# Optimization experiments

Measured on AMD Instinct MI355X. Metric: run time of the kernel, lower is better.

## Reference

```python
import jax, jax.numpy as jnp
import numpy as np

NUM_HEAD = 16
SIZE_PER_HEAD = 64
D_MODEL = NUM_HEAD * SIZE_PER_HEAD
BATCH = 4
SEQ = 2048
MASK_VAL = 1e10  # module uses 10000000000.0 for the causal mask


def setup_inputs() -> dict:
    key = jax.random.key(0)
    ks = jax.random.split(key, 11)
    s = 1.0 / np.sqrt(D_MODEL)
    return {
        "q": jax.random.normal(ks[0], (BATCH, SEQ, D_MODEL), jnp.float32),
        "k": jax.random.normal(ks[1], (BATCH, SEQ, D_MODEL), jnp.float32),
        "v": jax.random.normal(ks[2], (BATCH, SEQ, D_MODEL), jnp.float32),
        "WQ": jax.random.normal(ks[3], (D_MODEL, D_MODEL), jnp.float32) * s,
        "WQ_bias": jax.random.normal(ks[4], (D_MODEL,), jnp.float32) * 0.02,
        "WK": jax.random.normal(ks[5], (D_MODEL, D_MODEL), jnp.float32) * s,
        "WK_bias": jax.random.normal(ks[6], (D_MODEL,), jnp.float32) * 0.02,
        "WV": jax.random.normal(ks[7], (D_MODEL, D_MODEL), jnp.float32) * s,
        "WV_bias": jax.random.normal(ks[8], (D_MODEL,), jnp.float32) * 0.02,
        "WO": jax.random.normal(ks[9], (D_MODEL, D_MODEL), jnp.float32) * s,
        "WO_bias": jax.random.normal(ks[10], (D_MODEL,), jnp.float32) * 0.02,
    }


def _split_heads(x):
    # [B, S, H*D] -> [B, H, S, D]
    b, s, _ = x.shape
    return x.reshape(b, s, NUM_HEAD, SIZE_PER_HEAD).transpose(0, 2, 1, 3)


def reference(q, k, v, WQ, WQ_bias, WK, WK_bias, WV, WV_bias, WO, WO_bias):
    Q = _split_heads(q @ WQ + WQ_bias)  # [B,H,M,D]
    Kh = _split_heads(k @ WK + WK_bias)  # [B,H,N,D]
    Vh = _split_heads(v @ WV + WV_bias)  # [B,H,N,D]

    A = jnp.einsum('bhmd,bhnd->bhmn', Q, Kh)
    # causal mask (is_right=True): subtract 1e10 on strict upper triangle,
    # applied BEFORE the 1/sqrt(d) scale, exactly as the original.
    m, n = A.shape[-2], A.shape[-1]
    causal = jnp.triu(jnp.ones((m, n), A.dtype), k=1) * jnp.asarray(MASK_VAL, A.dtype)
    A = A - causal
    A = jax.nn.softmax(A / np.sqrt(SIZE_PER_HEAD).astype(np.float32), axis=-1)

    O = jnp.einsum('bhmn,bhnd->bhmd', A, Vh)  # [B,H,M,D]
    b, h, s, d = O.shape
    O = O.transpose(0, 2, 1, 3).reshape(b, s, h * d)
    return O @ WO + WO_bias
```

## Files before the change

### kernel.cpp

```cpp
#include <hip/hip_runtime.h>
#include <hip/hip_bf16.h>

typedef unsigned short u16;
typedef __attribute__((ext_vector_type(8))) short bf8_t;
typedef __attribute__((ext_vector_type(4))) float f4_t;
typedef __attribute__((ext_vector_type(2))) unsigned u32x2_t;
typedef __attribute__((ext_vector_type(4))) unsigned u32x4_t;

#define D_MODEL 1024
#define SEQ     2048
#define NHEAD   16
#define DH      64
#define MTOK    8192
#define ELEMS_PER_MAT 8388608

__device__ __forceinline__ u16 f2b(float x) {
    unsigned u = __float_as_uint(x);
    u += 0x7fffu + ((u >> 16) & 1u);
    return (u16)(u >> 16);
}

__device__ __forceinline__ unsigned pkrn(float lo, float hi) {
    __hip_bfloat162 h = __float22bfloat162_rn(make_float2(lo, hi));
    unsigned r;
    __builtin_memcpy(&r, &h, 4);
    return r;
}

__device__ __forceinline__ float ex2(float x) {
    float r;
    asm("v_exp_f32 %0, %1" : "=v"(r) : "v"(x));
    return r;
}

__device__ __forceinline__ void gl_lds16(const void* g, void* l) {
    __builtin_amdgcn_global_load_lds(
        (const __attribute__((address_space(1))) void*)g,
        (__attribute__((address_space(3))) void*)l, 16, 0, 0);
}

struct P3 { const float* p[3]; };
__global__ void cvt_in3(P3 src, u16* __restrict__ dst) {
    int z = blockIdx.y;
    const float* s = src.p[z];
    u16* d = dst + (size_t)z * ELEMS_PER_MAT;
    int i = blockIdx.x * 256 + threadIdx.x;
    const float4* s4 = (const float4*)s;
    float4 a = s4[i * 2];
    float4 b = s4[i * 2 + 1];
    bf8_t o;
    o[0] = (short)f2b(a.x); o[1] = (short)f2b(a.y);
    o[2] = (short)f2b(a.z); o[3] = (short)f2b(a.w);
    o[4] = (short)f2b(b.x); o[5] = (short)f2b(b.y);
    o[6] = (short)f2b(b.z); o[7] = (short)f2b(b.w);
    *(bf8_t*)&d[(size_t)i * 8] = o;
}

#define QSCALE 0.1803368801111244f
struct W4 { const float* w[4]; };
__global__ void cvt_wt(W4 wa, u16* __restrict__ wt) {
    int z = blockIdx.z;
    const float* W = wa.w[z];
    u16* Wt = wt + (size_t)z * 1048576;
    float scale = (z == 0) ? QSCALE : 1.0f;
    __shared__ float tl[64][65];
    int t = threadIdx.x;
    int bx = blockIdx.x, by = blockIdx.y;
#pragma unroll
    for (int i = 0; i < 16; i++) {
        int e = i * 256 + t;
        int row = e >> 6, col = e & 63;
        tl[row][col] = W[(size_t)(by * 64 + row) * 1024 + bx * 64 + col];
    }
    __syncthreads();
#pragma unroll
    for (int i = 0; i < 16; i++) {
        int e = i * 256 + t;
        int row = e >> 6, col = e & 63;
        Wt[(size_t)(bx * 64 + row) * 1024 + by * 64 + col] = f2b(tl[col][row] * scale);
    }
}

struct B4 { const float* b[4]; };
__global__ void cvt_bias(B4 ba, float* __restrict__ dst) {
    int t = threadIdx.x;
    for (int z = 0; z < 4; z++) {
        float sc = (z == 0) ? QSCALE : 1.0f;
        for (int i = t; i < 1024; i += 256) dst[z * 1024 + i] = ba.b[z][i] * sc;
    }
}

template <int MODE>
__global__ __launch_bounds__(256, 2) void gemm_k(const u16* __restrict__ Ab,
                                                 const u16* __restrict__ Btb,
                                                 const float* __restrict__ biasb,
                                                 void* __restrict__ out0,
                                                 u16* __restrict__ outV) {
    int z = blockIdx.z;
    const u16* A  = Ab  + (size_t)z * ELEMS_PER_MAT;
    const u16* Bt = Btb + (size_t)z * 1048576;
    const float* bias = biasb + z * 1024;
    bool vswap = (MODE == 3) && (z == 2);

    int bid = blockIdx.y * 64 + blockIdx.x;
    int xcd = bid & 7, seq = bid >> 3;
    int tm = xcd * 8 + (seq & 7);
    int tn = seq >> 3;
    int t = threadIdx.x;
    int wid = t >> 6, lane = t & 63;
    int wm = wid >> 1, wn = wid & 1;
    int la = lane & 15, lh = lane >> 4;

    __shared__ __align__(16) char smem[65536];

    f4_t acc[4][4];
#pragma unroll
    for (int m = 0; m < 4; m++)
#pragma unroll
        for (int n = 0; n < 4; n++) acc[m][n] = (f4_t){0.f, 0.f, 0.f, 0.f};

    const u16* Agb = A  + (size_t)(tm * 128) * 1024;
    const u16* Bgb = Bt + (size_t)(tn * 128) * 1024;

    int ch0 = wid * 64 + lane;
    int so0 = (lh ^ (la & 7)) * 8;
    int so1 = so0 ^ 32;

    auto stage = [&](int k0, int b) {
#pragma unroll
        for (int i = 0; i < 4; i++) {
            int ch = ch0 + i * 256;
            int row = ch >> 3, c8 = ch & 7;
            int srcc = (c8 ^ (row & 7)) * 8;
            gl_lds16(Agb + (size_t)row * 1024 + k0 + srcc,
                     smem + b * 32768 + (size_t)(i * 4 + wid) * 1024);
            gl_lds16(Bgb + (size_t)row * 1024 + k0 + srcc,
                     smem + b * 32768 + 16384 + (size_t)(i * 4 + wid) * 1024);
        }
    };

    stage(0, 0);
    __syncthreads();
    int cur = 0;
    for (int kt = 0; kt < 16; kt++) {
        if (kt + 1 < 16) stage((kt + 1) * 64, cur ^ 1);
        const u16* As = (const u16*)(smem + cur * 32768);
        const u16* Bs = (const u16*)(smem + cur * 32768 + 16384);
#pragma unroll
        for (int ks = 0; ks < 2; ks++) {
            int so = ks ? so1 : so0;
            bf8_t af[4], bf[4];
#pragma unroll
            for (int m = 0; m < 4; m++)
                af[m] = *(const bf8_t*)&As[(wm * 64 + m * 16 + la) * 64 + so];
#pragma unroll
            for (int n = 0; n < 4; n++)
                bf[n] = *(const bf8_t*)&Bs[(wn * 64 + n * 16 + la) * 64 + so];
            if (vswap) {
#pragma unroll
                for (int m = 0; m < 4; m++)
#pragma unroll
                    for (int n = 0; n < 4; n++)
                        acc[m][n] = __builtin_amdgcn_mfma_f32_16x16x32_bf16(bf[n], af[m], acc[m][n], 0, 0, 0);
            } else {
#pragma unroll
                for (int m = 0; m < 4; m++)
#pragma unroll
                    for (int n = 0; n < 4; n++)
                        acc[m][n] = __builtin_amdgcn_mfma_f32_16x16x32_bf16(af[m], bf[n], acc[m][n], 0, 0, 0);
            }
        }
        __syncthreads();
        cur ^= 1;
    }

    int lh4 = lh * 4;
    int bq = tm >> 4;
    int sloc = (tm & 15) * 128;

    if (MODE == 1) {
        float* ef = (float*)smem;
#pragma unroll
        for (int m = 0; m < 4; m++) {
            int row = wm * 64 + m * 16 + lh4;
#pragma unroll
            for (int n = 0; n < 4; n++) {
                int cb = wn * 64 + n * 16;
                float bv = bias[tn * 128 + cb + la];
#pragma unroll
                for (int r = 0; r < 4; r++)
                    ef[(row + r) * 128 + cb + la] = acc[m][n][r] + bv;
            }
        }
        __syncthreads();
        float* og = (float*)out0;
#pragma unroll
        for (int p = 0; p < 16; p++) {
            int e = t * 4 + p * 1024;
            int row = e >> 7, col = e & 127;
            f4_t v = *(const f4_t*)&ef[e];
            *(f4_t*)&og[(size_t)(tm * 128 + row) * 1024 + tn * 128 + col] = v;
        }
    } else if (vswap) {
        u16* eb = (u16*)smem;
#pragma unroll
        for (int m = 0; m < 4; m++) {
            int s = wm * 64 + m * 16 + la;
#pragma unroll
            for (int n = 0; n < 4; n++) {
                int cb = wn * 64 + n * 16 + lh4;
#pragma unroll
                for (int r = 0; r < 4; r++)
                    eb[(cb + r) * 128 + s] = f2b(acc[m][n][r] + bias[tn * 128 + cb + r]);
            }
        }
        __syncthreads();
#pragma unroll
        for (int p = 0; p < 8; p++) {
            int col = (t >> 4) + p * 16;
            int chunk = (t & 15) * 8;
            int h = tn * 2 + (col >> 6), d = col & 63;
            bf8_t v = *(const bf8_t*)&eb[col * 128 + chunk];
            *(bf8_t*)&outV[(((size_t)(bq * NHEAD + h)) * DH + d) * SEQ + sloc + chunk] = v;
        }
    } else {
        u16* eb = (u16*)smem;
#pragma unroll
        for (int m = 0; m < 4; m++) {
            int row = wm * 64 + m * 16 + lh4;
#pragma unroll
            for (int n = 0; n < 4; n++) {
                int cb = wn * 64 + n * 16;
                float bv = bias[tn * 128 + cb + la];
#pragma unroll
                for (int r = 0; r < 4; r++)
                    eb[wn * 8192 + (row + r) * 64 + n * 16 + la] = f2b(acc[m][n][r] + bv);
            }
        }
        __syncthreads();
        u16* outz = (u16*)out0 + (size_t)z * ELEMS_PER_MAT;
        size_t gbase = ((size_t)(bq * NHEAD + tn * 2) * SEQ + sloc) * DH;
#pragma unroll
        for (int p = 0; p < 8; p++) {
            int e = t * 8 + p * 2048;
            int hl = e >> 13, inner = e & 8191;
            bf8_t v = *(const bf8_t*)&eb[e];
            *(bf8_t*)&outz[gbase + (size_t)hl * SEQ * DH + inner] = v;
        }
    }
}

__global__ __launch_bounds__(256, 4) void attn(const u16* __restrict__ Qp,
                                               const u16* __restrict__ Kp,
                                               const u16* __restrict__ Vt,
                                               u16* __restrict__ ctx) {
    int id = blockIdx.x;
    int qt = 31 - (id >> 6);
    int bh = id & 63;
    int t = threadIdx.x, wid = t >> 6, lane = t & 63;
    int la = lane & 15, lh = lane >> 4;
    int lh4 = lh * 4;
    int lh8 = lh * 8;
    int q0 = qt * 64;

    const u16* Qb = Qp + (size_t)bh * SEQ * DH;
    const u16* Kb = Kp + (size_t)bh * SEQ * DH;
    const u16* Vb = Vt + (size_t)bh * DH * SEQ;

    __shared__ __align__(16) u16 Kl[2 * 4096];
    __shared__ __align__(16) u16 Vl[2 * 4096];

    int qrow = q0 + wid * 16 + la;
    bf8_t qf0 = *(const bf8_t*)&Qb[(size_t)qrow * DH + lh8];
    bf8_t qf1 = *(const bf8_t*)&Qb[(size_t)qrow * DH + 32 + lh8];

    bf8_t onesf;
#pragma unroll
    for (int i = 0; i < 8; i++) onesf[i] = (short)0x3F80;

    float m = -1e30f;
    f4_t o[4] = {};
    f4_t o5  = {};

    int s0 = t, s1 = t + 256;
    int rr0 = s0 >> 3, rr1 = s1 >> 3;
    int ck0 = ((s0 & 7) ^ (rr0 & 7)) * 8;
    int ck1 = ((s1 & 7) ^ (rr1 & 7)) * 8;
    int key0 = (rr0 & 0x23) | ((rr0 & 0x0C) << 1) | ((rr0 & 0x10) >> 2);
    int key1 = (rr1 & 0x23) | ((rr1 & 0x0C) << 1) | ((rr1 & 0x10) >> 2);
    const u16* kp0 = Kb + (size_t)key0 * DH + ck0;
    const u16* kp1 = Kb + (size_t)key1 * DH + ck1;
    const u16* vp0 = Vb + (size_t)rr0 * SEQ + ck0;
    const u16* vp1 = Vb + (size_t)rr1 * SEQ + ck1;

    int ntiles = qt + 1;
    auto stage = [&](int tile, int b) {
        int kv0 = tile * 64;
        gl_lds16(kp0 + (size_t)kv0 * DH, (char*)Kl + b * 8192 + wid * 1024);
        gl_lds16(kp1 + (size_t)kv0 * DH, (char*)Kl + b * 8192 + 4096 + wid * 1024);
        gl_lds16(vp0 + kv0,              (char*)Vl + b * 8192 + wid * 1024);
        gl_lds16(vp1 + kv0,              (char*)Vl + b * 8192 + 4096 + wid * 1024);
    };
    stage(0, 0);

    int csA = (lh ^ (la & 7)) * 8;
    int csB = ((4 | lh) ^ (la & 7)) * 8;

    for (int tkv = 0; tkv < ntiles; ++tkv) {
        __syncthreads();
        if (tkv + 1 < ntiles) stage(tkv + 1, (tkv + 1) & 1);
        const u16* Kd = Kl + (tkv & 1) * 4096;
        const u16* Vd = Vl + (tkv & 1) * 4096;

        bool diag = (tkv == qt);
        int ntmax = diag ? ((wid < 2) ? 2 : 4) : 4;

        f4_t st[4];
        __builtin_amdgcn_s_setprio(1);
#pragma unroll
        for (int nt = 0; nt < 4; nt++) {
            if (nt < ntmax) {
                bf8_t kf0 = *(const bf8_t*)&Kd[(nt * 16 + la) * 64 + csA];
                bf8_t kf1 = *(const bf8_t*)&Kd[(nt * 16 + la) * 64 + csB];
                f4_t a = (f4_t){0.f, 0.f, 0.f, 0.f};
                a = __builtin_amdgcn_mfma_f32_16x16x32_bf16(kf0, qf0, a, 0, 0, 0);
                a = __builtin_amdgcn_mfma_f32_16x16x32_bf16(kf1, qf1, a, 0, 0, 0);
                if (diag) {
                    int kbase = ((nt >> 1) << 5) + (lh << 3) + ((nt & 1) << 2);
#pragma unroll
                    for (int r = 0; r < 4; r++)
                        if (kbase + r > wid * 16 + la) a[r] = -1e30f;
                }
                st[nt] = a;
            } else {
                st[nt] = (f4_t){-1e30f, -1e30f, -1e30f, -1e30f};
            }
        }
        __builtin_amdgcn_s_setprio(0);

        float mloc = -3e38f;
#pragma unroll
        for (int nt = 0; nt < 4; nt++)
            if (nt < ntmax) {
                mloc = fmaxf(mloc, fmaxf(fmaxf(st[nt][0], st[nt][1]),
                                         fmaxf(st[nt][2], st[nt][3])));
            }
        mloc = fmaxf(mloc, __shfl_xor(mloc, 16));
        mloc = fmaxf(mloc, __shfl_xor(mloc, 32));
        if (!__all(mloc <= m + 8.0f)) {
            float mnew = fmaxf(m, mloc);
            float alpha = ex2(m - mnew);
#pragma unroll
            for (int dm = 0; dm < 4; dm++) o[dm] *= alpha;
            o5 *= alpha;
            m = mnew;
        }

#pragma unroll
        for (int nt = 0; nt < 4; nt++) {
#pragma unroll
            for (int r = 0; r < 4; r++)
                st[nt][r] = ex2(st[nt][r] - m);
        }

        __builtin_amdgcn_s_setprio(1);
#pragma unroll
        for (int kk = 0; kk < 2; kk++) {
            if (2 * kk < ntmax) {
                u32x4_t pw;
                pw[0] = pkrn(st[2 * kk][0], st[2 * kk][1]);
                pw[1] = pkrn(st[2 * kk][2], st[2 * kk][3]);
                pw[2] = pkrn(st[2 * kk + 1][0], st[2 * kk + 1][1]);
                pw[3] = pkrn(st[2 * kk + 1][2], st[2 * kk + 1][3]);
                bf8_t pf;
                __builtin_memcpy(&pf, &pw, 16);
                int cs = kk ? csB : csA;
#pragma unroll
                for (int dm = 0; dm < 4; dm++) {
                    bf8_t vf = *(const bf8_t*)&Vd[(dm * 16 + la) * 64 + cs];
                    o[dm] = __builtin_amdgcn_mfma_f32_16x16x32_bf16(vf, pf, o[dm], 0, 0, 0);
                }
                o5 = __builtin_amdgcn_mfma_f32_16x16x32_bf16(onesf, pf, o5, 0, 0, 0);
            }
        }
        __builtin_amdgcn_s_setprio(0);
    }

    float inv = 1.0f / o5[0];
    int b = bh >> 4, h = bh & 15;
    size_t base = ((size_t)(b * SEQ + qrow)) * D_MODEL + h * DH;
#pragma unroll
    for (int dm = 0; dm < 4; dm++) {
        u32x2_t w;
        w[0] = pkrn(o[dm][0] * inv, o[dm][1] * inv);
        w[1] = pkrn(o[dm][2] * inv, o[dm][3] * inv);
        *(u32x2_t*)&ctx[base + dm * 16 + lh4] = w;
    }
}

extern "C" void kernel_launch(void* const* d_in, const int* in_sizes, int n_in,
                              void* d_out, int out_size, void* d_ws, size_t ws_size,
                              hipStream_t stream) {
    const float* q   = (const float*)d_in[0];
    const float* k   = (const float*)d_in[1];
    const float* v   = (const float*)d_in[2];
    const float* WQ  = (const float*)d_in[3];
    const float* WQb = (const float*)d_in[4];
    const float* WK  = (const float*)d_in[5];
    const float* WKb = (const float*)d_in[6];
    const float* WV  = (const float*)d_in[7];
    const float* WVb = (const float*)d_in[8];
    const float* WO  = (const float*)d_in[9];
    const float* WOb = (const float*)d_in[10];

    char* ws = (char*)d_ws;
    u16*   qkv_bf = (u16*)(ws);
    u16*   Wt     = (u16*)(ws + 50331648);
    float* biasws = (float*)(ws + 58720256);
    u16*   QKVp   = (u16*)(ws + 58736640);
    u16*   Vt_    = (u16*)(ws + 109068288);
    u16*   ctx    = (u16*)(ws + 125845504);

    P3 p3; p3.p[0] = q; p3.p[1] = k; p3.p[2] = v;
    cvt_in3<<<dim3(4096, 3), 256, 0, stream>>>(p3, qkv_bf);

    W4 w4; w4.w[0] = WQ; w4.w[1] = WK; w4.w[2] = WV; w4.w[3] = WO;
    cvt_wt<<<dim3(16, 16, 4), 256, 0, stream>>>(w4, Wt);
    B4 b4; b4.b[0] = WQb; b4.b[1] = WKb; b4.b[2] = WVb; b4.b[3] = WOb;
    cvt_bias<<<1, 256, 0, stream>>>(b4, biasws);

    gemm_k<3><<<dim3(64, 8, 3), 256, 0, stream>>>(qkv_bf, Wt, biasws, QKVp, Vt_);

    attn<<<dim3(2048), 256, 0, stream>>>(QKVp, QKVp + ELEMS_PER_MAT, Vt_, ctx);

    gemm_k<1><<<dim3(64, 8, 1), 256, 0, stream>>>(ctx, Wt + 3 * 1048576,
                                                  biasws + 3 * 1024, d_out, nullptr);
}
```

Measured before the change: 183.2 us.

## Fuse fp32-to-bf16 input conversion into QKV projection GEMM A-tile loads

Removes the separate kernel that converted q/k/v from fp32 to bf16. The QKV GEMM now loads fp32 A tiles into registers, converts and packs them to bf16, and writes them swizzled into LDS after the MFMA work of the current tile. This drops one launch and the round trip of the bf16 copy through global memory. In exchange the GEMM reads twice as many bytes per A tile, uses more registers, and loses the direct global-to-LDS load path for A.

New measurement: 181.3 us. Within noise of the previous version (-1.1%).

```diff
diff --git a/kernel.cpp b/kernel.cpp
--- a/kernel.cpp
+++ b/kernel.cpp
@@ -40,21 +40,6 @@
 }
 
 struct P3 { const float* p[3]; };
-__global__ void cvt_in3(P3 src, u16* __restrict__ dst) {
-    int z = blockIdx.y;
-    const float* s = src.p[z];
-    u16* d = dst + (size_t)z * ELEMS_PER_MAT;
-    int i = blockIdx.x * 256 + threadIdx.x;
-    const float4* s4 = (const float4*)s;
-    float4 a = s4[i * 2];
-    float4 b = s4[i * 2 + 1];
-    bf8_t o;
-    o[0] = (short)f2b(a.x); o[1] = (short)f2b(a.y);
-    o[2] = (short)f2b(a.z); o[3] = (short)f2b(a.w);
-    o[4] = (short)f2b(b.x); o[5] = (short)f2b(b.y);
-    o[6] = (short)f2b(b.z); o[7] = (short)f2b(b.w);
-    *(bf8_t*)&d[(size_t)i * 8] = o;
-}
 
 #define QSCALE 0.1803368801111244f
 struct W4 { const float* w[4]; };
@@ -91,13 +76,14 @@
 }
 
 template <int MODE>
-__global__ __launch_bounds__(256, 2) void gemm_k(const u16* __restrict__ Ab,
+__global__ __launch_bounds__(256, 2) void gemm_k(P3 a3,
+                                                 const u16* __restrict__ Ab16,
                                                  const u16* __restrict__ Btb,
                                                  const float* __restrict__ biasb,
                                                  void* __restrict__ out0,
                                                  u16* __restrict__ outV) {
     int z = blockIdx.z;
-    const u16* A  = Ab  + (size_t)z * ELEMS_PER_MAT;
+    const float* Af = (MODE == 3) ? a3.p[z] : nullptr;
     const u16* Bt = Btb + (size_t)z * 1048576;
     const float* bias = biasb + z * 1024;
     bool vswap = (MODE == 3) && (z == 2);
@@ -119,14 +105,40 @@
 #pragma unroll
         for (int n = 0; n < 4; n++) acc[m][n] = (f4_t){0.f, 0.f, 0.f, 0.f};
 
-    const u16* Agb = A  + (size_t)(tm * 128) * 1024;
     const u16* Bgb = Bt + (size_t)(tn * 128) * 1024;
 
     int ch0 = wid * 64 + lane;
     int so0 = (lh ^ (la & 7)) * 8;
     int so1 = so0 ^ 32;
 
-    auto stage = [&](int k0, int b) {
+    f4_t areg[4][2];
+
+    auto aload = [&](int k0) {
+#pragma unroll
+        for (int i = 0; i < 4; i++) {
+            int ch = ch0 + i * 256;
+            int row = ch >> 3, c8 = ch & 7;
+            const float* src = Af + (size_t)(tm * 128 + row) * 1024 + k0 + c8 * 8;
+            areg[i][0] = *(const f4_t*)src;
+            areg[i][1] = *(const f4_t*)(src + 4);
+        }
+    };
+    auto awrite = [&](int b) {
+#pragma unroll
+        for (int i = 0; i < 4; i++) {
+            int ch = ch0 + i * 256;
+            int row = ch >> 3, c8 = ch & 7;
+            int slot = c8 ^ (row & 7);
+            u32x4_t w;
+            w[0] = pkrn(areg[i][0][0], areg[i][0][1]);
+            w[1] = pkrn(areg[i][0][2], areg[i][0][3]);
+            w[2] = pkrn(areg[i][1][0], areg[i][1][1]);
+            w[3] = pkrn(areg[i][1][2], areg[i][1][3]);
+            *(u32x4_t*)(smem + b * 32768 + (row * 8 + slot) * 16) = w;
+        }
+    };
+    auto astage16 = [&](int k0, int b) {
+        const u16* Agb = Ab16 + (size_t)(tm * 128) * 1024;
 #pragma unroll
         for (int i = 0; i < 4; i++) {
             int ch = ch0 + i * 256;
@@ -134,16 +146,29 @@
             int srcc = (c8 ^ (row & 7)) * 8;
             gl_lds16(Agb + (size_t)row * 1024 + k0 + srcc,
                      smem + b * 32768 + (size_t)(i * 4 + wid) * 1024);
+        }
+    };
+    auto bstage = [&](int k0, int b) {
+#pragma unroll
+        for (int i = 0; i < 4; i++) {
+            int ch = ch0 + i * 256;
+            int row = ch >> 3, c8 = ch & 7;
+            int srcc = (c8 ^ (row & 7)) * 8;
             gl_lds16(Bgb + (size_t)row * 1024 + k0 + srcc,
                      smem + b * 32768 + 16384 + (size_t)(i * 4 + wid) * 1024);
         }
     };
 
-    stage(0, 0);
+    if (MODE == 3) { aload(0); bstage(0, 0); awrite(0); }
+    else           { astage16(0, 0); bstage(0, 0); }
     __syncthreads();
+
     int cur = 0;
     for (int kt = 0; kt < 16; kt++) {
-        if (kt + 1 < 16) stage((kt + 1) * 64, cur ^ 1);
+        if (kt + 1 < 16) {
+            if (MODE == 3) { aload((kt + 1) * 64); bstage((kt + 1) * 64, cur ^ 1); }
+            else { astage16((kt + 1) * 64, cur ^ 1); bstage((kt + 1) * 64, cur ^ 1); }
+        }
         const u16* As = (const u16*)(smem + cur * 32768);
         const u16* Bs = (const u16*)(smem + cur * 32768 + 16384);
 #pragma unroll
@@ -170,6 +195,7 @@
                         acc[m][n] = __builtin_amdgcn_mfma_f32_16x16x32_bf16(af[m], bf[n], acc[m][n], 0, 0, 0);
             }
         }
+        if (MODE == 3 && kt + 1 < 16) awrite(cur ^ 1);
         __syncthreads();
         cur ^= 1;
     }
@@ -414,25 +440,23 @@
     const float* WOb = (const float*)d_in[10];
 
     char* ws = (char*)d_ws;
-    u16*   qkv_bf = (u16*)(ws);
     u16*   Wt     = (u16*)(ws + 50331648);
     float* biasws = (float*)(ws + 58720256);
     u16*   QKVp   = (u16*)(ws + 58736640);
     u16*   Vt_    = (u16*)(ws + 109068288);
     u16*   ctx    = (u16*)(ws + 125845504);
 
-    P3 p3; p3.p[0] = q; p3.p[1] = k; p3.p[2] = v;
-    cvt_in3<<<dim3(4096, 3), 256, 0, stream>>>(p3, qkv_bf);
-
     W4 w4; w4.w[0] = WQ; w4.w[1] = WK; w4.w[2] = WV; w4.w[3] = WO;
     cvt_wt<<<dim3(16, 16, 4), 256, 0, stream>>>(w4, Wt);
     B4 b4; b4.b[0] = WQb; b4.b[1] = WKb; b4.b[2] = WVb; b4.b[3] = WOb;
     cvt_bias<<<1, 256, 0, stream>>>(b4, biasws);
 
-    gemm_k<3><<<dim3(64, 8, 3), 256, 0, stream>>>(qkv_bf, Wt, biasws, QKVp, Vt_);
+    P3 a3; a3.p[0] = q; a3.p[1] = k; a3.p[2] = v;
+    gemm_k<3><<<dim3(64, 8, 3), 256, 0, stream>>>(a3, nullptr, Wt, biasws, QKVp, Vt_);
 
     attn<<<dim3(2048), 256, 0, stream>>>(QKVp, QKVp + ELEMS_PER_MAT, Vt_, ctx);
 
-    gemm_k<1><<<dim3(64, 8, 1), 256, 0, stream>>>(ctx, Wt + 3 * 1048576,
+    P3 dummy; dummy.p[0] = dummy.p[1] = dummy.p[2] = nullptr;
+    gemm_k<1><<<dim3(64, 8, 1), 256, 0, stream>>>(dummy, ctx, Wt + 3 * 1048576,
                                                   biasws + 3 * 1024, d_out, nullptr);
 }
```
